# Kernel tuning notes

Hardware: AMD Instinct MI355X
Metric: run time of the kernel (lower is better)

## Reference

```python
import jax, jax.numpy as jnp
import numpy as np

N_NODES = 50000
N_EDGES = 800000
D = 64  # out_dim


def setup_inputs() -> dict:
    key = jax.random.key(0)
    ks = jax.random.split(key, 9)
    K_h = jax.random.normal(ks[0], (N_NODES, D), dtype=jnp.float32)
    Q_h = jax.random.normal(ks[1], (N_NODES, D), dtype=jnp.float32)
    P_e = jax.random.normal(ks[2], (N_NODES, D), dtype=jnp.float32)
    src = jax.random.randint(ks[3], (N_EDGES,), 0, N_NODES, dtype=jnp.int32)
    dst = jax.random.randint(ks[4], (N_EDGES,), 0, N_NODES, dtype=jnp.int32)
    # MLP params: Linear(D, D) -> ReLU -> Linear(D, 1)
    lim1 = 1.0 / np.sqrt(D)
    W1 = jax.random.uniform(ks[5], (D, D), minval=-lim1, maxval=lim1, dtype=jnp.float32)
    b1 = jax.random.uniform(ks[6], (D,), minval=-lim1, maxval=lim1, dtype=jnp.float32)
    W2 = jax.random.uniform(ks[7], (D, 1), minval=-lim1, maxval=lim1, dtype=jnp.float32)
    b2 = jax.random.uniform(ks[8], (1,), minval=-lim1, maxval=lim1, dtype=jnp.float32)
    return {"K_h": K_h, "Q_h": Q_h, "P_e": P_e, "src": src, "dst": dst,
            "W1": W1, "b1": b1, "W2": W2, "b2": b2}


def reference(K_h, Q_h, P_e, src, dst, W1, b1, W2, b2):
    # Per-edge gather: src node K_h and P_e, dst node Q_h -> [E, D]
    dif = K_h[src] - Q_h[dst] + P_e[src]
    # Tiny 2-layer MLP per edge: [E, D] -> [E, D] -> [E, 1]
    h = jax.nn.relu(dif @ W1 + b1)
    score = h @ W2 + b2  # [E, 1]
    return score
```

## Files before the change

kernel.cpp:

```cpp
#include <hip/hip_runtime.h>
#include <hip/hip_fp16.h>

#define DD 64
#define NPB 64
#define LS 68

__global__ __launch_bounds__(256) void node_transform_kernel(
    const float* __restrict__ K_h, const float* __restrict__ Q_h,
    const float* __restrict__ P_e, const float* __restrict__ W1,
    const float* __restrict__ b1, __half* __restrict__ A,
    __half* __restrict__ Bm, int n_nodes)
{
    __shared__ float kpT[DD][LS];
    __shared__ float qT [DD][LS];
    __shared__ float ws [DD][DD];

    const int tid   = threadIdx.x;
    const int nbase = blockIdx.x * NPB;

    {
        const float4* w4 = (const float4*)W1;
        float4* s4 = (float4*)&ws[0][0];
#pragma unroll
        for (int j = 0; j < 4; ++j) {
            int idx = tid + j * 256;
            s4[idx] = w4[idx];
        }
    }

#pragma unroll
    for (int j = 0; j < 4; ++j) {
        int chunk = tid + j * 256;
        int r  = chunk >> 4;
        int k0 = (chunk & 15) << 2;
        int node = nbase + r;
        float4 kv = make_float4(0.f, 0.f, 0.f, 0.f);
        float4 pv = kv, qv = kv;
        if (node < n_nodes) {
            kv = *(const float4*)(K_h + (size_t)node * DD + k0);
            pv = *(const float4*)(P_e + (size_t)node * DD + k0);
            qv = *(const float4*)(Q_h + (size_t)node * DD + k0);
        }
        kpT[k0 + 0][r] = kv.x + pv.x;
        kpT[k0 + 1][r] = kv.y + pv.y;
        kpT[k0 + 2][r] = kv.z + pv.z;
        kpT[k0 + 3][r] = kv.w + pv.w;
        qT [k0 + 0][r] = qv.x;
        qT [k0 + 1][r] = qv.y;
        qT [k0 + 2][r] = qv.z;
        qT [k0 + 3][r] = qv.w;
    }
    __syncthreads();

    const int tx = tid & 15;
    const int ty = tid >> 4;
    const int c0 = tx * 4;
    const int r0 = ty * 4;

    float4 bv = *(const float4*)(b1 + c0);
    float accA[4][4], accB[4][4];
#pragma unroll
    for (int r = 0; r < 4; ++r) {
        accA[r][0] = bv.x; accA[r][1] = bv.y; accA[r][2] = bv.z; accA[r][3] = bv.w;
        accB[r][0] = 0.f;  accB[r][1] = 0.f;  accB[r][2] = 0.f;  accB[r][3] = 0.f;
    }

#pragma unroll 8
    for (int k = 0; k < DD; ++k) {
        float4 a4 = *(const float4*)&kpT[k][r0];
        float4 q4 = *(const float4*)&qT [k][r0];
        float4 w4 = *(const float4*)&ws [k][c0];
        const float av[4] = {a4.x, a4.y, a4.z, a4.w};
        const float qv[4] = {q4.x, q4.y, q4.z, q4.w};
        const float wv[4] = {w4.x, w4.y, w4.z, w4.w};
#pragma unroll
        for (int r = 0; r < 4; ++r) {
#pragma unroll
            for (int c = 0; c < 4; ++c) {
                accA[r][c] = fmaf(av[r], wv[c], accA[r][c]);
                accB[r][c] = fmaf(qv[r], wv[c], accB[r][c]);
            }
        }
    }

#pragma unroll
    for (int r = 0; r < 4; ++r) {
        int node = nbase + r0 + r;
        if (node >= n_nodes) continue;
        union { __half2 h[2]; float2 f; } ua, ub;
        ua.h[0] = __float22half2_rn(make_float2(accA[r][0], accA[r][1]));
        ua.h[1] = __float22half2_rn(make_float2(accA[r][2], accA[r][3]));
        ub.h[0] = __float22half2_rn(make_float2(accB[r][0], accB[r][1]));
        ub.h[1] = __float22half2_rn(make_float2(accB[r][2], accB[r][3]));
        *(float2*)(A  + (size_t)node * DD + c0) = ua.f;
        *(float2*)(Bm + (size_t)node * DD + c0) = ub.f;
    }
}

__global__ __launch_bounds__(256) void edge_score_kernel(
    const __half* __restrict__ A, const __half* __restrict__ Bm,
    const int* __restrict__ src, const int* __restrict__ dst,
    const float* __restrict__ W2, const float* __restrict__ b2,
    float* __restrict__ out, int n_edges)
{
    const int tid = threadIdx.x;
    const int g   = tid >> 3;
    const int c   = tid & 7;
    const int e0  = (blockIdx.x << 7) + (g << 2);
    if (e0 >= n_edges) return;

    float4 w0 = *(const float4*)(W2 + c * 8);
    float4 w1 = *(const float4*)(W2 + c * 8 + 4);
    const float wv[8] = {w0.x, w0.y, w0.z, w0.w, w1.x, w1.y, w1.z, w1.w};
    const size_t coff = (size_t)(c * 8);

    if (e0 + 3 < n_edges) {
        int4 sv = *(const int4*)(src + e0);
        int4 dv = *(const int4*)(dst + e0);

        float4 ra0 = *(const float4*)(A  + (size_t)sv.x * DD + coff);
        float4 rb0 = *(const float4*)(Bm + (size_t)dv.x * DD + coff);
        float4 ra1 = *(const float4*)(A  + (size_t)sv.y * DD + coff);
        float4 rb1 = *(const float4*)(Bm + (size_t)dv.y * DD + coff);
        float4 ra2 = *(const float4*)(A  + (size_t)sv.z * DD + coff);
        float4 rb2 = *(const float4*)(Bm + (size_t)dv.z * DD + coff);
        float4 ra3 = *(const float4*)(A  + (size_t)sv.w * DD + coff);
        float4 rb3 = *(const float4*)(Bm + (size_t)dv.w * DD + coff);

        float acc0 = 0.f, acc1 = 0.f, acc2 = 0.f, acc3 = 0.f;
        const __half2* ah0 = (const __half2*)&ra0;
        const __half2* bh0 = (const __half2*)&rb0;
        const __half2* ah1 = (const __half2*)&ra1;
        const __half2* bh1 = (const __half2*)&rb1;
        const __half2* ah2 = (const __half2*)&ra2;
        const __half2* bh2 = (const __half2*)&rb2;
        const __half2* ah3 = (const __half2*)&ra3;
        const __half2* bh3 = (const __half2*)&rb3;
#pragma unroll
        for (int j = 0; j < 4; ++j) {
            float2 x, y;
            x = __half22float2(ah0[j]); y = __half22float2(bh0[j]);
            acc0 = fmaf(fmaxf(x.x - y.x, 0.f), wv[2 * j + 0], acc0);
            acc0 = fmaf(fmaxf(x.y - y.y, 0.f), wv[2 * j + 1], acc0);
            x = __half22float2(ah1[j]); y = __half22float2(bh1[j]);
            acc1 = fmaf(fmaxf(x.x - y.x, 0.f), wv[2 * j + 0], acc1);
            acc1 = fmaf(fmaxf(x.y - y.y, 0.f), wv[2 * j + 1], acc1);
            x = __half22float2(ah2[j]); y = __half22float2(bh2[j]);
            acc2 = fmaf(fmaxf(x.x - y.x, 0.f), wv[2 * j + 0], acc2);
            acc2 = fmaf(fmaxf(x.y - y.y, 0.f), wv[2 * j + 1], acc2);
            x = __half22float2(ah3[j]); y = __half22float2(bh3[j]);
            acc3 = fmaf(fmaxf(x.x - y.x, 0.f), wv[2 * j + 0], acc3);
            acc3 = fmaf(fmaxf(x.y - y.y, 0.f), wv[2 * j + 1], acc3);
        }

        acc0 += __shfl_xor(acc0, 1); acc1 += __shfl_xor(acc1, 1);
        acc2 += __shfl_xor(acc2, 1); acc3 += __shfl_xor(acc3, 1);
        acc0 += __shfl_xor(acc0, 2); acc1 += __shfl_xor(acc1, 2);
        acc2 += __shfl_xor(acc2, 2); acc3 += __shfl_xor(acc3, 2);
        acc0 += __shfl_xor(acc0, 4); acc1 += __shfl_xor(acc1, 4);
        acc2 += __shfl_xor(acc2, 4); acc3 += __shfl_xor(acc3, 4);

        if (c == 0) {
            float bb = b2[0];
            *(float4*)(out + e0) =
                make_float4(acc0 + bb, acc1 + bb, acc2 + bb, acc3 + bb);
        }
    } else {
        for (int e = e0; e < n_edges && e < e0 + 4; ++e) {
            int s = src[e], d = dst[e];
            float4 ar = *(const float4*)(A  + (size_t)s * DD + coff);
            float4 br = *(const float4*)(Bm + (size_t)d * DD + coff);
            const __half2* ah = (const __half2*)&ar;
            const __half2* bh = (const __half2*)&br;
            float acc = 0.f;
#pragma unroll
            for (int j = 0; j < 4; ++j) {
                float2 x = __half22float2(ah[j]);
                float2 y = __half22float2(bh[j]);
                acc = fmaf(fmaxf(x.x - y.x, 0.f), wv[2 * j + 0], acc);
                acc = fmaf(fmaxf(x.y - y.y, 0.f), wv[2 * j + 1], acc);
            }
            acc += __shfl_xor(acc, 1);
            acc += __shfl_xor(acc, 2);
            acc += __shfl_xor(acc, 4);
            if (c == 0) out[e] = acc + b2[0];
        }
    }
}

extern "C" void kernel_launch(void* const* d_in, const int* in_sizes, int n_in,
                              void* d_out, int out_size, void* d_ws, size_t ws_size,
                              hipStream_t stream) {
    const float* K_h = (const float*)d_in[0];
    const float* Q_h = (const float*)d_in[1];
    const float* P_e = (const float*)d_in[2];
    const int*   src = (const int*)d_in[3];
    const int*   dst = (const int*)d_in[4];
    const float* W1  = (const float*)d_in[5];
    const float* b1  = (const float*)d_in[6];
    const float* W2  = (const float*)d_in[7];
    const float* b2  = (const float*)d_in[8];
    float* out = (float*)d_out;

    int n_nodes = in_sizes[0] / DD;
    int n_edges = in_sizes[3];

    __half* A  = (__half*)d_ws;
    __half* Bm = A + (size_t)n_nodes * DD;

    node_transform_kernel<<<(n_nodes + NPB - 1) / NPB, 256, 0, stream>>>(
        K_h, Q_h, P_e, W1, b1, A, Bm, n_nodes);
    edge_score_kernel<<<(n_edges + 127) / 128, 256, 0, stream>>>(
        A, Bm, src, dst, W2, b2, out, n_edges);
}
```

Measured before the change: 131.3 us.

## Compute node transform GEMM with fp16 MFMA instead of scalar FMA

Replaces the scalar fp32 register-tiled GEMM in the node transform kernel with MFMA 16x16x32 fp16 instructions. Inputs and a transposed W1 are staged in shared memory as fp16 rather than fp32. Outputs are written with per-element half stores in the MFMA output layout. This lowers ALU cost for the node stage, but rounds the GEMM inputs to fp16 (lower precision) and uses narrower, less coalesced global stores. The edge kernel, which likely dominates runtime, is unchanged.

```diff
diff --git a/kernel.cpp b/kernel.cpp
--- a/kernel.cpp
+++ b/kernel.cpp
@@ -3,97 +3,97 @@
 
 #define DD 64
 #define NPB 64
-#define LS 68
-
-__global__ __launch_bounds__(256) void node_transform_kernel(
+#define LP 72
+
+typedef _Float16 f16x8 __attribute__((ext_vector_type(8)));
+typedef float    f32x4 __attribute__((ext_vector_type(4)));
+
+__global__ __launch_bounds__(256) void node_transform_mfma(
     const float* __restrict__ K_h, const float* __restrict__ Q_h,
     const float* __restrict__ P_e, const float* __restrict__ W1,
     const float* __restrict__ b1, __half* __restrict__ A,
     __half* __restrict__ Bm, int n_nodes)
 {
-    __shared__ float kpT[DD][LS];
-    __shared__ float qT [DD][LS];
-    __shared__ float ws [DD][DD];
+    __shared__ __half XH [NPB][LP];
+    __shared__ __half QH [NPB][LP];
+    __shared__ __half W1T[DD][LP];
 
     const int tid   = threadIdx.x;
     const int nbase = blockIdx.x * NPB;
 
     {
-        const float4* w4 = (const float4*)W1;
-        float4* s4 = (float4*)&ws[0][0];
-#pragma unroll
-        for (int j = 0; j < 4; ++j) {
-            int idx = tid + j * 256;
-            s4[idx] = w4[idx];
-        }
-    }
-
-#pragma unroll
-    for (int j = 0; j < 4; ++j) {
-        int chunk = tid + j * 256;
-        int r  = chunk >> 4;
-        int k0 = (chunk & 15) << 2;
+        const int k  = tid >> 2;
+        const int n0 = (tid & 3) << 4;
+        const float* wr = W1 + k * DD + n0;
+        float4 w0 = *(const float4*)(wr);
+        float4 w1v = *(const float4*)(wr + 4);
+        float4 w2v = *(const float4*)(wr + 8);
+        float4 w3v = *(const float4*)(wr + 12);
+        const float wv[16] = {w0.x,w0.y,w0.z,w0.w, w1v.x,w1v.y,w1v.z,w1v.w,
+                              w2v.x,w2v.y,w2v.z,w2v.w, w3v.x,w3v.y,w3v.z,w3v.w};
+#pragma unroll
+        for (int j = 0; j < 16; ++j)
+            W1T[n0 + j][k] = __float2half(wv[j]);
+    }
+
+#pragma unroll
+    for (int ch = 0; ch < 4; ++ch) {
+        int idx = tid + (ch << 8);
+        int r   = idx >> 4;
+        int q4  = idx & 15;
         int node = nbase + r;
-        float4 kv = make_float4(0.f, 0.f, 0.f, 0.f);
+        float4 kv = make_float4(0.f,0.f,0.f,0.f);
         float4 pv = kv, qv = kv;
         if (node < n_nodes) {
-            kv = *(const float4*)(K_h + (size_t)node * DD + k0);
-            pv = *(const float4*)(P_e + (size_t)node * DD + k0);
-            qv = *(const float4*)(Q_h + (size_t)node * DD + k0);
-        }
-        kpT[k0 + 0][r] = kv.x + pv.x;
-        kpT[k0 + 1][r] = kv.y + pv.y;
-        kpT[k0 + 2][r] = kv.z + pv.z;
-        kpT[k0 + 3][r] = kv.w + pv.w;
-        qT [k0 + 0][r] = qv.x;
-        qT [k0 + 1][r] = qv.y;
-        qT [k0 + 2][r] = qv.z;
-        qT [k0 + 3][r] = qv.w;
+            kv = *(const float4*)(K_h + (size_t)node * DD + q4 * 4);
+            pv = *(const float4*)(P_e + (size_t)node * DD + q4 * 4);
+            qv = *(const float4*)(Q_h + (size_t)node * DD + q4 * 4);
+        }
+        __half2* xh = (__half2*)&XH[r][q4 << 2];
+        xh[0] = __float22half2_rn(make_float2(kv.x + pv.x, kv.y + pv.y));
+        xh[1] = __float22half2_rn(make_float2(kv.z + pv.z, kv.w + pv.w));
+        __half2* qh = (__half2*)&QH[r][q4 << 2];
+        qh[0] = __float22half2_rn(make_float2(qv.x, qv.y));
+        qh[1] = __float22half2_rn(make_float2(qv.z, qv.w));
     }
     __syncthreads();
 
-    const int tx = tid & 15;
-    const int ty = tid >> 4;
-    const int c0 = tx * 4;
-    const int r0 = ty * 4;
-
-    float4 bv = *(const float4*)(b1 + c0);
-    float accA[4][4], accB[4][4];
+    const int w    = tid >> 6;
+    const int lane = tid & 63;
+    const int m    = lane & 15;
+    const int q    = lane >> 4;
+    const int row  = (w << 4) + m;
+
+    f16x8 xlo = *(const f16x8*)&XH[row][(q << 3)];
+    f16x8 xhi = *(const f16x8*)&XH[row][32 + (q << 3)];
+    f16x8 qlo = *(const f16x8*)&QH[row][(q << 3)];
+    f16x8 qhi = *(const f16x8*)&QH[row][32 + (q << 3)];
+
+    f32x4 accA[4], accB[4];
+#pragma unroll
+    for (int t = 0; t < 4; ++t) {
+        float bb = b1[t * 16 + m];
+        accA[t] = (f32x4){bb, bb, bb, bb};
+        accB[t] = (f32x4){0.f, 0.f, 0.f, 0.f};
+        f16x8 wlo = *(const f16x8*)&W1T[t * 16 + m][(q << 3)];
+        f16x8 whi = *(const f16x8*)&W1T[t * 16 + m][32 + (q << 3)];
+        accA[t] = __builtin_amdgcn_mfma_f32_16x16x32_f16(xlo, wlo, accA[t], 0, 0, 0);
+        accA[t] = __builtin_amdgcn_mfma_f32_16x16x32_f16(xhi, whi, accA[t], 0, 0, 0);
+        accB[t] = __builtin_amdgcn_mfma_f32_16x16x32_f16(qlo, wlo, accB[t], 0, 0, 0);
+        accB[t] = __builtin_amdgcn_mfma_f32_16x16x32_f16(qhi, whi, accB[t], 0, 0, 0);
+    }
+
 #pragma unroll
     for (int r = 0; r < 4; ++r) {
-        accA[r][0] = bv.x; accA[r][1] = bv.y; accA[r][2] = bv.z; accA[r][3] = bv.w;
-        accB[r][0] = 0.f;  accB[r][1] = 0.f;  accB[r][2] = 0.f;  accB[r][3] = 0.f;
-    }
-
-#pragma unroll 8
-    for (int k = 0; k < DD; ++k) {
-        float4 a4 = *(const float4*)&kpT[k][r0];
-        float4 q4 = *(const float4*)&qT [k][r0];
-        float4 w4 = *(const float4*)&ws [k][c0];
-        const float av[4] = {a4.x, a4.y, a4.z, a4.w};
-        const float qv[4] = {q4.x, q4.y, q4.z, q4.w};
-        const float wv[4] = {w4.x, w4.y, w4.z, w4.w};
-#pragma unroll
-        for (int r = 0; r < 4; ++r) {
-#pragma unroll
-            for (int c = 0; c < 4; ++c) {
-                accA[r][c] = fmaf(av[r], wv[c], accA[r][c]);
-                accB[r][c] = fmaf(qv[r], wv[c], accB[r][c]);
-            }
-        }
-    }
-
-#pragma unroll
-    for (int r = 0; r < 4; ++r) {
-        int node = nbase + r0 + r;
+        int node = nbase + (w << 4) + (q << 2) + r;
         if (node >= n_nodes) continue;
-        union { __half2 h[2]; float2 f; } ua, ub;
-        ua.h[0] = __float22half2_rn(make_float2(accA[r][0], accA[r][1]));
-        ua.h[1] = __float22half2_rn(make_float2(accA[r][2], accA[r][3]));
-        ub.h[0] = __float22half2_rn(make_float2(accB[r][0], accB[r][1]));
-        ub.h[1] = __float22half2_rn(make_float2(accB[r][2], accB[r][3]));
-        *(float2*)(A  + (size_t)node * DD + c0) = ua.f;
-        *(float2*)(Bm + (size_t)node * DD + c0) = ub.f;
+        __half* Arow = A  + (size_t)node * DD + m;
+        __half* Brow = Bm + (size_t)node * DD + m;
+#pragma unroll
+        for (int t = 0; t < 4; ++t) {
+            Arow[t * 16] = __float2half(accA[t][r]);
+            Brow[t * 16] = __float2half(accB[t][r]);
+        }
     }
 }
 
@@ -208,7 +208,7 @@
     __half* A  = (__half*)d_ws;
     __half* Bm = A + (size_t)n_nodes * DD;
 
-    node_transform_kernel<<<(n_nodes + NPB - 1) / NPB, 256, 0, stream>>>(
+    node_transform_mfma<<<(n_nodes + NPB - 1) / NPB, 256, 0, stream>>>(
         K_h, Q_h, P_e, W1, b1, A, Bm, n_nodes);
     edge_score_kernel<<<(n_edges + 127) / 128, 256, 0, stream>>>(
         A, Bm, src, dst, W2, b2, out, n_edges);
```

Measured after the change: 121.3 us. -7.6%, faster.
